# Kernel tuning notes

Hardware: AMD Instinct MI355X
Metric: run time of the kernel (lower is better)

The kernel has to match this reference:

```python
import jax, jax.numpy as jnp
import numpy as np


def setup_inputs() -> dict:
    key = jax.random.key(0)
    ks = jax.random.split(key, 7)
    B, S, D, F, E = 4, 2048, 1024, 4096, 8
    scale = 0.02
    return {
        "x": jax.random.normal(ks[0], (B, S, D), dtype=jnp.float32),
        "gate_w": jax.random.normal(ks[1], (D, E), dtype=jnp.float32) * scale,
        "gate_b": jnp.zeros((E,), dtype=jnp.float32),
        "w1": jax.random.normal(ks[2], (E, D, F), dtype=jnp.float32) * scale,
        "b1": jnp.zeros((E, F), dtype=jnp.float32),
        "w2": jax.random.normal(ks[3], (E, F, D), dtype=jnp.float32) * scale,
        "b2": jnp.zeros((E, D), dtype=jnp.float32),
        "top_k": 2,
    }


def reference(x, gate_w, gate_b, w1, b1, w2, b2, top_k):
    B, S, D = x.shape
    E = w1.shape[0]
    xf = x.reshape(-1, D)                      # [T, D], T = B*S
    T = xf.shape[0]

    # Router: top-k logits, softmax over the selected k (as in torch code)
    logits = xf @ gate_w + gate_b              # [T, E]
    rw, sel = jax.lax.top_k(logits, top_k)     # [T, k], [T, k]
    w = jax.nn.softmax(rw, axis=-1)            # [T, k]

    # Dense combine weights: combine[t, e] = sum_k w[t,k] * (sel[t,k]==e)
    combine = jnp.zeros((T, E), dtype=xf.dtype)
    combine = combine.at[jnp.arange(T)[:, None], sel].add(w)

    # Loop over small fixed expert count; each expert FFN on all tokens,
    # weighted by combine (zero for unrouted tokens). Dropout p honored as 0 (eval).
    out = jnp.zeros_like(xf)
    for e in range(E):
        h = jax.nn.gelu(xf @ w1[e] + b1[e], approximate=False)  # torch F.gelu = exact
        out = out + combine[:, e:e + 1] * (h @ w2[e] + b2[e])
    return out.reshape(B, S, D)
```

## Files before the change

kernel.cpp:

```cpp
#include <hip/hip_runtime.h>
#include <math.h>

#define T_TOK 8192
#define DDIM  1024
#define FDIM  4096
#define NEXP  8
#define MAXT  136
#define NSLOT (2 * T_TOK)
#define NG1   (32 * MAXT)
#define NG2   (2 * 8 * MAXT)

typedef __attribute__((ext_vector_type(8))) short short8;
typedef __attribute__((ext_vector_type(4))) float f32x4;
typedef unsigned short u16;
typedef unsigned int   u32;

typedef const __attribute__((address_space(1))) u32* gp_t;
typedef       __attribute__((address_space(3))) u32* lp_t;

__device__ __forceinline__ void gload16(const void* g, void* l) {
  __builtin_amdgcn_global_load_lds((gp_t)g, (lp_t)l, 16, 0, 0);
}

__device__ __forceinline__ u16 f2bf(float f) {
  u32 u = __float_as_uint(f);
  u = u + 0x7FFFu + ((u >> 16) & 1u);
  return (u16)(u >> 16);
}

__device__ __forceinline__ int imin(int a, int b) { return a < b ? a : b; }

__device__ __forceinline__ float gelu_fast(float v) {
  float u = 0.7978845608f * (v + 0.044715f * v * v * v);
  float t2 = __expf(2.f * u);
  float th = 1.f - 2.f / (t2 + 1.f);
  return 0.5f * v * (1.f + th);
}

__device__ __forceinline__ int xcd_swz(int orig, int nwg) {
  int xcd = orig & 7;
  int q = nwg >> 3, r = nwg & 7;
  int base = (xcd < r) ? xcd * (q + 1) : r * (q + 1) + (xcd - r) * q;
  return base + (orig >> 3);
}

__global__ __launch_bounds__(256) void router_kernel(
    const float* __restrict__ x, const float* __restrict__ gw,
    const float* __restrict__ gb,
    int* __restrict__ counts, int* __restrict__ sel, float* __restrict__ wts)
{
  const int t    = blockIdx.x * 4 + (threadIdx.x >> 6);
  const int lane = threadIdx.x & 63;
  const float* xr = x + (size_t)t * DDIM;
  float lg[NEXP];
  #pragma unroll
  for (int e = 0; e < NEXP; e++) lg[e] = 0.f;
  #pragma unroll
  for (int i = 0; i < 4; i++) {
    int d0 = i * 256 + lane * 4;
    float4 v = *(const float4*)(xr + d0);
    const float* g = gw + (size_t)d0 * NEXP;
    #pragma unroll
    for (int e = 0; e < NEXP; e++)
      lg[e] += v.x * g[e] + v.y * g[NEXP + e] + v.z * g[2 * NEXP + e] + v.w * g[3 * NEXP + e];
  }
  #pragma unroll
  for (int off = 32; off > 0; off >>= 1) {
    #pragma unroll
    for (int e = 0; e < NEXP; e++) lg[e] += __shfl_down(lg[e], off);
  }
  if (lane == 0) {
    float v0 = -1e30f, v1 = -1e30f; int s0 = 0, s1 = 0;
    #pragma unroll
    for (int e = 0; e < NEXP; e++) {
      float v = lg[e] + gb[e];
      if (v > v0) { v1 = v0; s1 = s0; v0 = v; s0 = e; }
      else if (v > v1) { v1 = v; s1 = e; }
    }
    float a  = expf(v1 - v0);
    float w0 = 1.f / (1.f + a);
    sel[t * 2] = s0; sel[t * 2 + 1] = s1;
    wts[t * 2] = w0; wts[t * 2 + 1] = 1.f - w0;
    atomicAdd(&counts[s0], 1); atomicAdd(&counts[s1], 1);
  }
}

__global__ __launch_bounds__(256) void scan_assign_kernel(
    const int* __restrict__ counts, const int* __restrict__ sel,
    const float* __restrict__ wts,
    int* __restrict__ offsets, int* __restrict__ map_e, int* __restrict__ map_r,
    int* __restrict__ nT, int* __restrict__ stok, float* __restrict__ swgt)
{
  __shared__ int spos[NEXP];
  if (threadIdx.x == 0) {
    int run = 0, nt = 0;
    for (int e = 0; e < NEXP; e++) {
      offsets[e] = run; spos[e] = run;
      int c = counts[e];
      int ntile = (c + 127) >> 7;
      for (int i = 0; i < ntile; i++) { map_e[nt] = e; map_r[nt] = i * 128; nt++; }
      run += c;
    }
    nT[0] = nt;
  }
  __syncthreads();
  for (int t = threadIdx.x; t < T_TOK; t += 256) {
    #pragma unroll
    for (int k = 0; k < 2; k++) {
      int e = sel[t * 2 + k];
      int p = atomicAdd(&spos[e], 1);
      stok[p] = t; swgt[p] = wts[t * 2 + k];
    }
  }
}

__global__ __launch_bounds__(256) void xgather_kernel(
    const float* __restrict__ x, const int* __restrict__ stok,
    u16* __restrict__ Xg)
{
  const int s = blockIdx.x;
  int tok = stok[s]; if ((u32)tok >= T_TOK) tok = 0;
  float4 v = *(const float4*)(x + (size_t)tok * DDIM + threadIdx.x * 4);
  ushort4 o;
  o.x = f2bf(v.x); o.y = f2bf(v.y); o.z = f2bf(v.z); o.w = f2bf(v.w);
  *(ushort4*)(Xg + (size_t)s * DDIM + threadIdx.x * 4) = o;
}

__device__ void wtrans_tile(float* __restrict__ tile,
                            const float* __restrict__ in, u16* __restrict__ out,
                            int M, int N, int r0, int c0)
{
  const int tid = threadIdx.x;
  const int tr = tid >> 4, tc = (tid & 15) * 4;
  #pragma unroll
  for (int p = 0; p < 4; p++) {
    int r = p * 16 + tr;
    float4 v = *(const float4*)(in + (size_t)(r0 + r) * N + (c0 + tc));
    tile[r * 65 + tc]     = v.x; tile[r * 65 + tc + 1] = v.y;
    tile[r * 65 + tc + 2] = v.z; tile[r * 65 + tc + 3] = v.w;
  }
  __syncthreads();
  const int oc = tid >> 3, om = (tid & 7) * 8;
  #pragma unroll
  for (int p = 0; p < 2; p++) {
    int c = p * 32 + oc;
    short8 o;
    #pragma unroll
    for (int j = 0; j < 8; j++) o[j] = (short)f2bf(tile[(om + j) * 65 + c]);
    *(short8*)(out + (size_t)(c0 + c) * M + (r0 + om)) = o;
  }
}

__global__ __launch_bounds__(256) void wtrans_all_kernel(
    const float* __restrict__ w1, u16* __restrict__ w1t,
    const float* __restrict__ w2, u16* __restrict__ w2t)
{
  __shared__ __align__(16) float tile[64 * 65];
  const int t = blockIdx.x;
  if (t < 8192) {
    int e = t >> 10, rem = t & 1023;
    int tm = rem >> 4, tn = rem & 15;
    wtrans_tile(tile, w2 + (size_t)e * FDIM * DDIM,
                w2t + (size_t)e * FDIM * DDIM, FDIM, DDIM, tm * 64, tn * 64);
  } else {
    int tt = t - 8192;
    int e = tt >> 10, rem = tt & 1023;
    int tn = rem >> 4, tm = rem & 15;
    wtrans_tile(tile, w1 + (size_t)e * DDIM * FDIM,
                w1t + (size_t)e * DDIM * FDIM, DDIM, FDIM, tm * 64, tn * 64);
  }
}

__global__ __launch_bounds__(256) void gemm1_kernel(
    const u16* __restrict__ Xg, const u16* __restrict__ W1T,
    const float* __restrict__ B1,
    const int* __restrict__ counts, const int* __restrict__ offsets,
    const int* __restrict__ map_e, const int* __restrict__ map_r,
    const int* __restrict__ nT, u16* __restrict__ H)
{
  __shared__ __align__(16) char lds[16384];
  const int L     = xcd_swz(blockIdx.x, NG1);
  const int xg    = L / 544;
  const int local = L - xg * 544;
  const int tl    = local >> 5;
  const int n_idx = local & 31;
  const int t_idx = xg * 17 + tl;
  if (t_idx >= nT[0]) return;
  const int e    = map_e[t_idx];
  const int row0 = map_r[t_idx];
  const int cnt  = counts[e];
  const int off  = offsets[e];
  const int n0   = n_idx * 128;

  u16* As = (u16*)lds;
  u16* Bs = (u16*)(lds + 8192);
  const int tid = threadIdx.x, wave = tid >> 6, lane = tid & 63;
  const int lr = lane & 15, lq = lane >> 4;
  const int wr = wave >> 1, wc = wave & 1;
  const int l2 = lane >> 2, lb = (lane & 3) * 16;

  const char* gA[2]; const char* gB[2];
  #pragma unroll
  for (int i = 0; i < 2; i++) {
    int R = (wave * 2 + i) * 16 + l2;
    int aidx = imin(off + row0 + R, NSLOT - 1);
    gA[i] = (const char*)Xg + (size_t)aidx * 2048 + lb;
    gB[i] = (const char*)W1T + (size_t)(e * FDIM + n0 + R) * 2048 + lb;
  }

  f32x4 acc[4][4] = {};
  #pragma unroll 1
  for (int k0 = 0; k0 < 2048; k0 += 64) {
    __syncthreads();
    gload16(gA[0] + k0, lds + (wave * 2) * 1024 + lane * 16);
    gload16(gA[1] + k0, lds + (wave * 2 + 1) * 1024 + lane * 16);
    gload16(gB[0] + k0, lds + 8192 + (wave * 2) * 1024 + lane * 16);
    gload16(gB[1] + k0, lds + 8192 + (wave * 2 + 1) * 1024 + lane * 16);
    __syncthreads();
    short8 a[4], bf[4];
    #pragma unroll
    for (int m = 0; m < 4; m++)
      a[m] = *(const short8*)&As[(wr * 64 + m * 16 + lr) * 32 + lq * 8];
    #pragma unroll
    for (int n = 0; n < 4; n++)
      bf[n] = *(const short8*)&Bs[(wc * 64 + n * 16 + lr) * 32 + lq * 8];
    #pragma unroll
    for (int m = 0; m < 4; m++)
      #pragma unroll
      for (int n = 0; n < 4; n++)
        acc[m][n] = __builtin_amdgcn_mfma_f32_16x16x32_bf16(a[m], bf[n], acc[m][n], 0, 0, 0);
  }

  #pragma unroll
  for (int nn = 0; nn < 4; nn++) {
    int col = n0 + wc * 64 + nn * 16 + lr;
    float b1v = B1[e * FDIM + col];
    #pragma unroll
    for (int m = 0; m < 4; m++) {
      int rbase = wr * 64 + m * 16 + lq * 4;
      #pragma unroll
      for (int j = 0; j < 4; j++) {
        int r = rbase + j;
        if (row0 + r < cnt) {
          float v = acc[m][nn][j] + b1v;
          H[(size_t)(off + row0 + r) * FDIM + col] = f2bf(gelu_fast(v));
        }
      }
    }
  }
}

__global__ __launch_bounds__(256) void gemm2_kernel(
    const u16* __restrict__ H, const u16* __restrict__ W2T,
    const float* __restrict__ B2,
    const int* __restrict__ counts, const int* __restrict__ offsets,
    const int* __restrict__ slot_token, const float* __restrict__ slot_weight,
    const int* __restrict__ map_e, const int* __restrict__ map_r,
    const int* __restrict__ nT, float* __restrict__ out)
{
  __shared__ __align__(16) char lds[16384];
  const int L     = xcd_swz(blockIdx.x, NG2);
  const int xg    = L / 272;
  const int local = L - xg * 272;
  const int tl    = local >> 4;
  const int combo = local & 15;
  const int sp    = combo >> 3;
  const int n_idx = combo & 7;
  const int t_idx = xg * 17 + tl;
  if (t_idx >= nT[0]) return;
  const int e    = map_e[t_idx];
  const int row0 = map_r[t_idx];
  const int cnt  = counts[e];
  const int off  = offsets[e];
  const int n0   = n_idx * 128;
  const int kbase = sp * 4096;

  u16* As = (u16*)lds;
  u16* Bs = (u16*)(lds + 8192);
  const int tid = threadIdx.x, wave = tid >> 6, lane = tid & 63;
  const int lr = lane & 15, lq = lane >> 4;
  const int wr = wave >> 1, wc = wave & 1;
  const int l2 = lane >> 2, lb = (lane & 3) * 16;

  const char* gA[2]; const char* gB[2];
  #pragma unroll
  for (int i = 0; i < 2; i++) {
    int R = (wave * 2 + i) * 16 + l2;
    int aidx = imin(off + row0 + R, NSLOT - 1);
    gA[i] = (const char*)H + (size_t)aidx * 8192 + kbase + lb;
    gB[i] = (const char*)W2T + (size_t)(e * DDIM + n0 + R) * 8192 + kbase + lb;
  }

  f32x4 acc[4][4] = {};
  #pragma unroll 1
  for (int k0 = 0; k0 < 4096; k0 += 64) {
    __syncthreads();
    gload16(gA[0] + k0, lds + (wave * 2) * 1024 + lane * 16);
    gload16(gA[1] + k0, lds + (wave * 2 + 1) * 1024 + lane * 16);
    gload16(gB[0] + k0, lds + 8192 + (wave * 2) * 1024 + lane * 16);
    gload16(gB[1] + k0, lds + 8192 + (wave * 2 + 1) * 1024 + lane * 16);
    __syncthreads();
    short8 a[4], bf[4];
    #pragma unroll
    for (int m = 0; m < 4; m++)
      a[m] = *(const short8*)&As[(wr * 64 + m * 16 + lr) * 32 + lq * 8];
    #pragma unroll
    for (int n = 0; n < 4; n++)
      bf[n] = *(const short8*)&Bs[(wc * 64 + n * 16 + lr) * 32 + lq * 8];
    #pragma unroll
    for (int m = 0; m < 4; m++)
      #pragma unroll
      for (int n = 0; n < 4; n++)
        acc[m][n] = __builtin_amdgcn_mfma_f32_16x16x32_bf16(a[m], bf[n], acc[m][n], 0, 0, 0);
  }

  #pragma unroll
  for (int m = 0; m < 4; m++) {
    int rbase = wr * 64 + m * 16 + lq * 4;
    #pragma unroll
    for (int j = 0; j < 4; j++) {
      int r = rbase + j;
      if (row0 + r >= cnt) continue;
      int s = off + row0 + r;
      int tok = slot_token[s];
      float wgt = slot_weight[s];
      #pragma unroll
      for (int n = 0; n < 4; n++) {
        int col = n0 + wc * 64 + n * 16 + lr;
        float v = acc[m][n][j];
        if (sp == 0) v += B2[e * DDIM + col];
        atomicAdd(&out[(size_t)tok * DDIM + col], wgt * v);
      }
    }
  }
}

extern "C" void kernel_launch(void* const* d_in, const int* in_sizes, int n_in,
                              void* d_out, int out_size, void* d_ws, size_t ws_size,
                              hipStream_t stream)
{
  (void)in_sizes; (void)n_in; (void)ws_size;
  const float* x  = (const float*)d_in[0];
  const float* gw = (const float*)d_in[1];
  const float* gb = (const float*)d_in[2];
  const float* w1 = (const float*)d_in[3];
  const float* b1 = (const float*)d_in[4];
  const float* w2 = (const float*)d_in[5];
  const float* b2 = (const float*)d_in[6];

  char* ws = (char*)d_ws;
  int*   counts = (int*)(ws + 0);
  int*   offp   = (int*)(ws + 64);
  int*   nT     = (int*)(ws + 128);
  int*   map_e  = (int*)(ws + 256);
  int*   map_r  = (int*)(ws + 1024);

  size_t p = 2048;
  int*   sel   = (int*)(ws + p);   p += (size_t)T_TOK * 2 * 4;
  float* wts   = (float*)(ws + p); p += (size_t)T_TOK * 2 * 4;
  int*   stok  = (int*)(ws + p);   p += (size_t)NSLOT * 4;
  float* swgt  = (float*)(ws + p); p += (size_t)NSLOT * 4;
  p = (p + 1048575) & ~(size_t)1048575;
  u16*   Xg    = (u16*)(ws + p);   p += (size_t)NSLOT * DDIM * 2;
  u16*   w1t   = (u16*)(ws + p);   p += (size_t)NEXP * DDIM * FDIM * 2;
  u16*   w2t   = (u16*)(ws + p);   p += (size_t)NEXP * DDIM * FDIM * 2;
  u16*   Hbuf  = (u16*)(ws + p);

  hipMemsetAsync(ws, 0, 256, stream);
  hipMemsetAsync(d_out, 0, (size_t)out_size * sizeof(float), stream);
  router_kernel<<<T_TOK / 4, 256, 0, stream>>>(x, gw, gb, counts, sel, wts);
  scan_assign_kernel<<<1, 256, 0, stream>>>(counts, sel, wts, offp, map_e, map_r, nT, stok, swgt);
  xgather_kernel<<<NSLOT, 256, 0, stream>>>(x, stok, Xg);
  wtrans_all_kernel<<<16384, 256, 0, stream>>>(w1, w1t, w2, w2t);
  gemm1_kernel<<<NG1, 256, 0, stream>>>(
      Xg, w1t, b1, counts, offp, map_e, map_r, nT, Hbuf);
  gemm2_kernel<<<NG2, 256, 0, stream>>>(
      Hbuf, w2t, b2, counts, offp, stok, swgt, map_e, map_r, nT, (float*)d_out);
}
```

Baseline: 909.0 us.

## Use 256-row tiles with 8 waves and double-buffered LDS prefetch in expert GEMMs

Both expert GEMMs move from 128x128 tiles on 4 waves to 256x128 tiles on 8 waves, so each weight tile loaded into LDS is reused across twice as many token rows. The k-loop now double-buffers LDS: the next K-slab is issued with global_load_lds before computing on the current one, and one waitcnt plus barrier replaces the two syncthreads. Routing tile maps are rebuilt at 256-row granularity. This adds LDS per block and more padded rows for experts whose counts are not multiples of 256.

After: 870.0 us. -4.3%, faster.

```diff
diff --git a/kernel.cpp b/kernel.cpp
--- a/kernel.cpp
+++ b/kernel.cpp
@@ -5,10 +5,10 @@
 #define DDIM  1024
 #define FDIM  4096
 #define NEXP  8
-#define MAXT  136
+#define MT256 72
 #define NSLOT (2 * T_TOK)
-#define NG1   (32 * MAXT)
-#define NG2   (2 * 8 * MAXT)
+#define NG1   (32 * MT256)
+#define NG2   (16 * MT256)
 
 typedef __attribute__((ext_vector_type(8))) short short8;
 typedef __attribute__((ext_vector_type(4))) float f32x4;
@@ -21,6 +21,10 @@
 __device__ __forceinline__ void gload16(const void* g, void* l) {
   __builtin_amdgcn_global_load_lds((gp_t)g, (lp_t)l, 16, 0, 0);
 }
+
+#define VM0 asm volatile("s_waitcnt vmcnt(0)" ::: "memory")
+#define SBAR __builtin_amdgcn_s_barrier()
+#define SCHED0 __builtin_amdgcn_sched_barrier(0)
 
 __device__ __forceinline__ u16 f2bf(float f) {
   u32 u = __float_as_uint(f);
@@ -97,8 +101,8 @@
     for (int e = 0; e < NEXP; e++) {
       offsets[e] = run; spos[e] = run;
       int c = counts[e];
-      int ntile = (c + 127) >> 7;
-      for (int i = 0; i < ntile; i++) { map_e[nt] = e; map_r[nt] = i * 128; nt++; }
+      int ntile = (c + 255) >> 8;
+      for (int i = 0; i < ntile; i++) { map_e[nt] = e; map_r[nt] = i * 256; nt++; }
       run += c;
     }
     nT[0] = nt;
@@ -171,20 +175,20 @@
   }
 }
 
-__global__ __launch_bounds__(256) void gemm1_kernel(
+__global__ __launch_bounds__(512, 4) void gemm1_kernel(
     const u16* __restrict__ Xg, const u16* __restrict__ W1T,
     const float* __restrict__ B1,
     const int* __restrict__ counts, const int* __restrict__ offsets,
     const int* __restrict__ map_e, const int* __restrict__ map_r,
     const int* __restrict__ nT, u16* __restrict__ H)
 {
-  __shared__ __align__(16) char lds[16384];
+  __shared__ __align__(16) char lds[2 * 24576];
   const int L     = xcd_swz(blockIdx.x, NG1);
-  const int xg    = L / 544;
-  const int local = L - xg * 544;
+  const int xg    = L / 288;
+  const int local = L - xg * 288;
   const int tl    = local >> 5;
   const int n_idx = local & 31;
-  const int t_idx = xg * 17 + tl;
+  const int t_idx = xg * 9 + tl;
   if (t_idx >= nT[0]) return;
   const int e    = map_e[t_idx];
   const int row0 = map_r[t_idx];
@@ -192,31 +196,34 @@
   const int off  = offsets[e];
   const int n0   = n_idx * 128;
 
-  u16* As = (u16*)lds;
-  u16* Bs = (u16*)(lds + 8192);
   const int tid = threadIdx.x, wave = tid >> 6, lane = tid & 63;
   const int lr = lane & 15, lq = lane >> 4;
   const int wr = wave >> 1, wc = wave & 1;
   const int l2 = lane >> 2, lb = (lane & 3) * 16;
 
-  const char* gA[2]; const char* gB[2];
+  const char* gA[2]; const char* gB;
   #pragma unroll
   for (int i = 0; i < 2; i++) {
     int R = (wave * 2 + i) * 16 + l2;
     int aidx = imin(off + row0 + R, NSLOT - 1);
     gA[i] = (const char*)Xg + (size_t)aidx * 2048 + lb;
-    gB[i] = (const char*)W1T + (size_t)(e * FDIM + n0 + R) * 2048 + lb;
-  }
+  }
+  {
+    int R = wave * 16 + l2;
+    gB = (const char*)W1T + (size_t)(e * FDIM + n0 + R) * 2048 + lb;
+  }
+
+  auto stage = [&](int buf, int k0) {
+    char* base = lds + buf * 24576;
+    gload16(gA[0] + k0, base + (wave * 2) * 1024 + lane * 16);
+    gload16(gA[1] + k0, base + (wave * 2 + 1) * 1024 + lane * 16);
+    gload16(gB + k0, base + 16384 + wave * 1024 + lane * 16);
+  };
 
   f32x4 acc[4][4] = {};
-  #pragma unroll 1
-  for (int k0 = 0; k0 < 2048; k0 += 64) {
-    __syncthreads();
-    gload16(gA[0] + k0, lds + (wave * 2) * 1024 + lane * 16);
-    gload16(gA[1] + k0, lds + (wave * 2 + 1) * 1024 + lane * 16);
-    gload16(gB[0] + k0, lds + 8192 + (wave * 2) * 1024 + lane * 16);
-    gload16(gB[1] + k0, lds + 8192 + (wave * 2 + 1) * 1024 + lane * 16);
-    __syncthreads();
+  auto compute = [&](int buf) {
+    const u16* As = (const u16*)(lds + buf * 24576);
+    const u16* Bs = (const u16*)(lds + buf * 24576 + 16384);
     short8 a[4], bf[4];
     #pragma unroll
     for (int m = 0; m < 4; m++)
@@ -229,6 +236,15 @@
       #pragma unroll
       for (int n = 0; n < 4; n++)
         acc[m][n] = __builtin_amdgcn_mfma_f32_16x16x32_bf16(a[m], bf[n], acc[m][n], 0, 0, 0);
+  };
+
+  stage(0, 0);
+  VM0; SCHED0; SBAR; SCHED0;
+  #pragma unroll 1
+  for (int t = 0; t < 32; t++) {
+    if (t < 31) stage((t + 1) & 1, (t + 1) * 64);
+    compute(t & 1);
+    SCHED0; VM0; SCHED0; SBAR; SCHED0;
   }
 
   #pragma unroll
@@ -250,7 +266,7 @@
   }
 }
 
-__global__ __launch_bounds__(256) void gemm2_kernel(
+__global__ __launch_bounds__(512, 4) void gemm2_kernel(
     const u16* __restrict__ H, const u16* __restrict__ W2T,
     const float* __restrict__ B2,
     const int* __restrict__ counts, const int* __restrict__ offsets,
@@ -258,15 +274,15 @@
     const int* __restrict__ map_e, const int* __restrict__ map_r,
     const int* __restrict__ nT, float* __restrict__ out)
 {
-  __shared__ __align__(16) char lds[16384];
+  __shared__ __align__(16) char lds[2 * 24576];
   const int L     = xcd_swz(blockIdx.x, NG2);
-  const int xg    = L / 272;
-  const int local = L - xg * 272;
+  const int xg    = L / 144;
+  const int local = L - xg * 144;
   const int tl    = local >> 4;
   const int combo = local & 15;
   const int sp    = combo >> 3;
   const int n_idx = combo & 7;
-  const int t_idx = xg * 17 + tl;
+  const int t_idx = xg * 9 + tl;
   if (t_idx >= nT[0]) return;
   const int e    = map_e[t_idx];
   const int row0 = map_r[t_idx];
@@ -275,31 +291,34 @@
   const int n0   = n_idx * 128;
   const int kbase = sp * 4096;
 
-  u16* As = (u16*)lds;
-  u16* Bs = (u16*)(lds + 8192);
   const int tid = threadIdx.x, wave = tid >> 6, lane = tid & 63;
   const int lr = lane & 15, lq = lane >> 4;
   const int wr = wave >> 1, wc = wave & 1;
   const int l2 = lane >> 2, lb = (lane & 3) * 16;
 
-  const char* gA[2]; const char* gB[2];
+  const char* gA[2]; const char* gB;
   #pragma unroll
   for (int i = 0; i < 2; i++) {
     int R = (wave * 2 + i) * 16 + l2;
     int aidx = imin(off + row0 + R, NSLOT - 1);
     gA[i] = (const char*)H + (size_t)aidx * 8192 + kbase + lb;
-    gB[i] = (const char*)W2T + (size_t)(e * DDIM + n0 + R) * 8192 + kbase + lb;
-  }
+  }
+  {
+    int R = wave * 16 + l2;
+    gB = (const char*)W2T + (size_t)(e * DDIM + n0 + R) * 8192 + kbase + lb;
+  }
+
+  auto stage = [&](int buf, int k0) {
+    char* base = lds + buf * 24576;
+    gload16(gA[0] + k0, base + (wave * 2) * 1024 + lane * 16);
+    gload16(gA[1] + k0, base + (wave * 2 + 1) * 1024 + lane * 16);
+    gload16(gB + k0, base + 16384 + wave * 1024 + lane * 16);
+  };
 
   f32x4 acc[4][4] = {};
-  #pragma unroll 1
-  for (int k0 = 0; k0 < 4096; k0 += 64) {
-    __syncthreads();
-    gload16(gA[0] + k0, lds + (wave * 2) * 1024 + lane * 16);
-    gload16(gA[1] + k0, lds + (wave * 2 + 1) * 1024 + lane * 16);
-    gload16(gB[0] + k0, lds + 8192 + (wave * 2) * 1024 + lane * 16);
-    gload16(gB[1] + k0, lds + 8192 + (wave * 2 + 1) * 1024 + lane * 16);
-    __syncthreads();
+  auto compute = [&](int buf) {
+    const u16* As = (const u16*)(lds + buf * 24576);
+    const u16* Bs = (const u16*)(lds + buf * 24576 + 16384);
     short8 a[4], bf[4];
     #pragma unroll
     for (int m = 0; m < 4; m++)
@@ -312,6 +331,15 @@
       #pragma unroll
       for (int n = 0; n < 4; n++)
         acc[m][n] = __builtin_amdgcn_mfma_f32_16x16x32_bf16(a[m], bf[n], acc[m][n], 0, 0, 0);
+  };
+
+  stage(0, 0);
+  VM0; SCHED0; SBAR; SCHED0;
+  #pragma unroll 1
+  for (int t = 0; t < 64; t++) {
+    if (t < 63) stage((t + 1) & 1, (t + 1) * 64);
+    compute(t & 1);
+    SCHED0; VM0; SCHED0; SBAR; SCHED0;
   }
 
   #pragma unroll
@@ -372,8 +400,8 @@
   scan_assign_kernel<<<1, 256, 0, stream>>>(counts, sel, wts, offp, map_e, map_r, nT, stok, swgt);
   xgather_kernel<<<NSLOT, 256, 0, stream>>>(x, stok, Xg);
   wtrans_all_kernel<<<16384, 256, 0, stream>>>(w1, w1t, w2, w2t);
-  gemm1_kernel<<<NG1, 256, 0, stream>>>(
+  gemm1_kernel<<<NG1, 512, 0, stream>>>(
       Xg, w1t, b1, counts, offp, map_e, map_r, nT, Hbuf);
-  gemm2_kernel<<<NG2, 256, 0, stream>>>(
+  gemm2_kernel<<<NG2, 512, 0, stream>>>(
       Hbuf, w2t, b2, counts, offp, stok, swgt, map_e, map_r, nT, (float*)d_out);
 }
```
